# Optimization experiments

Hardware: AMD Instinct MI355X
Metric: run time of the kernel (lower is better)

Reference implementation:

```python
import jax, jax.numpy as jnp
import numpy as np

DIM = 256
HEADS = 8
WS = 7          # window size
SS = 3          # shift size
B = 16
HIMG = 56
WIMG = 56
N = WS * WS     # tokens per window = 49
HID = DIM * 4


def _rel_index(ws):
    coords = np.stack(np.meshgrid(np.arange(ws), np.arange(ws), indexing='ij')).reshape(2, -1)
    rel = (coords[:, :, None] - coords[:, None, :]).transpose(1, 2, 0)
    rel[:, :, 0] += ws - 1
    rel[:, :, 1] += ws - 1
    rel[:, :, 0] *= 2 * ws - 1
    return rel.sum(-1)  # (N, N) int

REL_IDX = jnp.asarray(_rel_index(WS))


def _make_attn_mask(H, W, ws, ss):
    img = np.zeros((H, W), dtype=np.float32)
    cnt = 0
    for hs in (slice(0, -ws), slice(-ws, -ss), slice(-ss, None)):
        for wsl in (slice(0, -ws), slice(-ws, -ss), slice(-ss, None)):
            img[hs, wsl] = cnt
            cnt += 1
    mw = img.reshape(H // ws, ws, W // ws, ws).transpose(0, 2, 1, 3).reshape(-1, ws * ws)
    diff = mw[:, None, :] - mw[:, :, None]  # (nW, N, N)
    return jnp.asarray(np.where(diff != 0, -100.0, 0.0).astype(np.float32))


def _layernorm(x, g, b):
    m = jnp.mean(x, -1, keepdims=True)
    v = jnp.mean((x - m) ** 2, -1, keepdims=True)
    return (x - m) / jnp.sqrt(v + 1e-5) * g + b


def _win_part(x, ws):
    Bb, H, W, C = x.shape
    x = x.reshape(Bb, H // ws, ws, W // ws, ws, C).transpose(0, 1, 3, 2, 4, 5)
    return x.reshape(-1, ws * ws, C)  # (B*nW, N, C)


def _win_rev(w, ws, H, W):
    C = w.shape[-1]
    Bb = w.shape[0] // ((H // ws) * (W // ws))
    x = w.reshape(Bb, H // ws, W // ws, ws, ws, C).transpose(0, 1, 3, 2, 4, 5)
    return x.reshape(Bb, H, W, C)


def setup_inputs() -> dict:
    key = jax.random.key(0)
    ks = jax.random.split(key, 20)
    n = lambda k, s, sc=0.02: jax.random.normal(k, s, dtype=jnp.float32) * sc
    inp = {
        'x1': jax.random.normal(ks[0], (B, HIMG * WIMG, DIM), dtype=jnp.float32),
        'x2': jax.random.normal(ks[1], (B, HIMG * WIMG, DIM), dtype=jnp.float32),
        'x3': jax.random.normal(ks[2], (B, HIMG * WIMG, DIM), dtype=jnp.float32),
        'attn_mask': _make_attn_mask(HIMG, WIMG, WS, SS),
        'g1': jnp.ones((DIM,), jnp.float32), 'bb1': jnp.zeros((DIM,), jnp.float32),
        'wq': n(ks[3], (DIM, DIM)), 'bq': jnp.zeros((DIM,), jnp.float32),
        'wk': n(ks[4], (DIM, DIM)), 'bk': jnp.zeros((DIM,), jnp.float32),
        'wv': n(ks[5], (DIM, DIM)), 'bv': jnp.zeros((DIM,), jnp.float32),
        'rel_table': n(ks[6], ((2 * WS - 1) ** 2, HEADS)),
        'wp': n(ks[7], (DIM, DIM)), 'bp': jnp.zeros((DIM,), jnp.float32),
        'g2': jnp.ones((DIM,), jnp.float32), 'bb2': jnp.zeros((DIM,), jnp.float32),
        'fw1': n(ks[8], (DIM, HID)), 'fb1': jnp.zeros((HID,), jnp.float32),
        'fw2': n(ks[9], (HID, DIM)), 'fb2': jnp.zeros((DIM,), jnp.float32),
        'H': HIMG, 'W': WIMG,
    }
    return inp


def reference(x1, x2, x3, attn_mask, g1, bb1, wq, bq, wk, bk, wv, bv, rel_table,
              wp, bp, g2, bb2, fw1, fb1, fw2, fb2, H, W):
    Bb, L, C = x1.shape
    hd = C // HEADS
    shortcut = x1

    def prep(x):
        x = _layernorm(x, g1, bb1).reshape(Bb, H, W, C)
        return jnp.roll(x, (-SS, -SS), axis=(1, 2))  # cyclic shift (shift_size>0)

    xw1 = _win_part(prep(x1), WS)  # (B*nW, N, C)
    xw2 = _win_part(prep(x2), WS)
    xw3 = _win_part(prep(x3), WS)

    def to_heads(x, w, b):
        y = x @ w + b
        return y.reshape(-1, N, HEADS, hd).transpose(0, 2, 1, 3)  # (B_, h, N, hd)

    q = to_heads(xw1, wq, bq) * (hd ** -0.5)
    k = to_heads(xw2, wk, bk)
    v = to_heads(xw3, wv, bv)

    attn = jnp.einsum('bhnd,bhmd->bhnm', q, k)  # (B_, h, N, N)
    bias = rel_table[REL_IDX].transpose(2, 0, 1)  # (h, N, N) gather
    attn = attn + bias[None]
    nW = attn_mask.shape[0]
    attn = attn.reshape(Bb, nW, HEADS, N, N) + attn_mask[None, :, None]
    attn = jax.nn.softmax(attn.reshape(-1, HEADS, N, N), axis=-1)

    out = jnp.einsum('bhnm,bhmd->bhnd', attn, v).transpose(0, 2, 1, 3).reshape(-1, N, C)
    out = out @ wp + bp

    x = _win_rev(out, WS, H, W)
    x = jnp.roll(x, (SS, SS), axis=(1, 2)).reshape(Bb, L, C)  # reverse shift

    x = shortcut + x
    h = jax.nn.gelu(_layernorm(x, g2, bb2) @ fw1 + fb1, approximate=False) @ fw2 + fb2
    return x + h
```

## Files before the change

### kernel.cpp

```cpp
#include <hip/hip_runtime.h>

typedef unsigned short u16;
typedef short bf16x8 __attribute__((ext_vector_type(8)));
typedef float f32x4 __attribute__((ext_vector_type(4)));

__device__ __forceinline__ u16 f2bf(float f) {
  union { float f; unsigned u; } x; x.f = f;
  unsigned r = x.u + 0x7FFFu + ((x.u >> 16) & 1u);
  return (u16)(r >> 16);
}
__device__ __forceinline__ float gelu_f(float x) {
  float t = 0.7978845608028654f * x * (1.f + 0.044715f * x * x);
  return x / (1.f + __expf(-2.f * t));
}
__device__ __forceinline__ void gll16(const void* g, void* l) {
  __builtin_amdgcn_global_load_lds(
      (const __attribute__((address_space(1))) unsigned int*)g,
      (__attribute__((address_space(3))) unsigned int*)l, 16, 0, 0);
}
__device__ __forceinline__ size_t winmap(int t) {
  int win = t / 49, i = t - win * 49;
  int b = win >> 6, wi = win & 63;
  int ih = i / 7, iw = i - ih * 7;
  int h2 = (wi >> 3) * 7 + ih + 3; if (h2 >= 56) h2 -= 56;
  int w2 = (wi & 7) * 7 + iw + 3; if (w2 >= 56) w2 -= 56;
  return ((size_t)b * 3136 + (size_t)h2 * 56 + w2) * 256;
}

__global__ __launch_bounds__(256)
void prep_all(const float* __restrict__ wq, const float* __restrict__ wk,
              const float* __restrict__ wv, const float* __restrict__ wp,
              const float* __restrict__ fw1, const float* __restrict__ fw2,
              u16* __restrict__ wqt, u16* __restrict__ wkt,
              u16* __restrict__ wvt, u16* __restrict__ wpt,
              u16* __restrict__ fw1t, u16* __restrict__ fw2t,
              const float* __restrict__ rel, const float* __restrict__ mask,
              float* __restrict__ Bp) {
  const int bx = blockIdx.x;
  const int tid = threadIdx.x;
  if (bx >= 192) {
    const int blk = bx - 192;
    const int wi = blk >> 3, h = blk & 7;
    const float* mrow = mask + (size_t)wi * 2401;
    float* ob = Bp + (size_t)blk * 4096;
#pragma unroll
    for (int e = 0; e < 16; ++e) {
      int pos = e * 256 + tid;
      int r = pos & 3, lane = (pos >> 2) & 63, mini = pos >> 8;
      int mi = mini >> 2, ni = mini & 3;
      int row = mi * 16 + (lane >> 4) * 4 + r;
      int col = ni * 16 + (lane & 15);
      float val;
      if (col >= 49) val = -1e30f;
      else if (row >= 49) val = 0.f;
      else {
        int idx = (row / 7 - col / 7 + 6) * 13 + (row % 7 - col % 7 + 6);
        val = rel[idx * 8 + h] + mrow[row * 49 + col];
      }
      ob[pos] = val;
    }
    return;
  }
  const float* in; u16* out; int K, N, t;
  if (bx < 64) {
    int j = bx >> 4; t = bx & 15; K = 256; N = 256;
    in = j == 0 ? wq : (j == 1 ? wk : (j == 2 ? wv : wp));
    out = j == 0 ? wqt : (j == 1 ? wkt : (j == 2 ? wvt : wpt));
  } else if (bx < 128) {
    t = bx - 64; in = fw1; out = fw1t; K = 256; N = 1024;
  } else {
    t = bx - 128; in = fw2; out = fw2t; K = 1024; N = 256;
  }
  const int ntn = N >> 6;
  const int tk = t / ntn, tn = t - tk * ntn;
  __shared__ u16 tile[64][72];
#pragma unroll
  for (int it = 0; it < 4; ++it) {
    int G = it * 256 + tid;
    int kk = G >> 4, gg = G & 15;
    float4 v = *(const float4*)(in + (size_t)(tk * 64 + kk) * N + tn * 64 + gg * 4);
    tile[kk][gg * 4 + 0] = f2bf(v.x);
    tile[kk][gg * 4 + 1] = f2bf(v.y);
    tile[kk][gg * 4 + 2] = f2bf(v.z);
    tile[kk][gg * 4 + 3] = f2bf(v.w);
  }
  __syncthreads();
#pragma unroll
  for (int it = 0; it < 4; ++it) {
    int G = it * 256 + tid;
    int nn = G >> 4, gk = G & 15;
    ushort4 o;
    o.x = tile[gk * 4 + 0][nn];
    o.y = tile[gk * 4 + 1][nn];
    o.z = tile[gk * 4 + 2][nn];
    o.w = tile[gk * 4 + 3][nn];
    *(ushort4*)(out + (size_t)(tn * 64 + nn) * K + tk * 64 + gk * 4) = o;
  }
}

template <int EPI, int QKV>
__global__ __launch_bounds__(256, 4)
void gemm_k256(const float* __restrict__ X0, const float* __restrict__ X1,
               const float* __restrict__ X2, const float* __restrict__ lng,
               const float* __restrict__ lnb, const u16* __restrict__ Abf,
               const u16* __restrict__ Bt, const float* __restrict__ b0,
               const float* __restrict__ b1, const float* __restrict__ b2,
               float alpha, int NC, int N, void* __restrict__ out_,
               const float* __restrict__ res) {
  __shared__ __align__(16) u16 Bl[2][32 * 256];
  const int tid = threadIdx.x, lane = tid & 63, wave = tid >> 6;
  const int q = lane >> 4, m = lane & 15;
  const int wm = wave >> 1, wn = wave & 1;
  const float* bias = b0;
  float al = alpha;
  size_t aoff = 0;
  const float* xsrc = X0;
  if constexpr (QKV) {
    const int y = blockIdx.y;
    aoff = (size_t)y * 12845056;
    Bt += (size_t)y * 65536;
    bias = (y == 0) ? b0 : (y == 1 ? b1 : b2);
    if (y) al = 1.f;
    xsrc = (y == 0) ? X0 : (y == 1 ? X1 : X2);
  }
  const long rowBase = (long)blockIdx.x * 64;

  bf16x8 af[2][8];
  if constexpr (QKV) {
    u16* Abuf = (u16*)Bl;
    const float4 gv = *(const float4*)(lng + lane * 4);
    const float4 bv = *(const float4*)(lnb + lane * 4);
#pragma unroll
    for (int pp = 0; pp < 16; ++pp) {
      int lrow = wave * 16 + pp;
      size_t src = winmap((int)(rowBase + lrow));
      float4 v = *(const float4*)(xsrc + src + lane * 4);
      float sm = v.x + v.y + v.z + v.w;
      float s2 = v.x * v.x + v.y * v.y + v.z * v.z + v.w * v.w;
#pragma unroll
      for (int d = 32; d > 0; d >>= 1) {
        sm += __shfl_xor(sm, d);
        s2 += __shfl_xor(s2, d);
      }
      float mean = sm * (1.f / 256.f);
      float rstd = rsqrtf(s2 * (1.f / 256.f) - mean * mean + 1e-5f);
      ushort4 ov;
      ov.x = f2bf((v.x - mean) * rstd * gv.x + bv.x);
      ov.y = f2bf((v.y - mean) * rstd * gv.y + bv.y);
      ov.z = f2bf((v.z - mean) * rstd * gv.z + bv.z);
      ov.w = f2bf((v.w - mean) * rstd * gv.w + bv.w);
      int g = lane >> 1;
      int gs = (g & ~7) | ((g & 7) ^ (lrow & 7));
      *(ushort4*)&Abuf[lrow * 256 + gs * 8 + (lane & 1) * 4] = ov;
    }
    __syncthreads();
#pragma unroll
    for (int mt = 0; mt < 2; ++mt) {
      int row = wm * 32 + mt * 16 + m;
#pragma unroll
      for (int ks = 0; ks < 8; ++ks) {
        int g = ks * 4 + q;
        int gs = (g & ~7) | ((g & 7) ^ (row & 7));
        af[mt][ks] = *(const bf16x8*)&Abuf[row * 256 + gs * 8];
      }
    }
    __syncthreads();
  } else {
#pragma unroll
    for (int mt = 0; mt < 2; ++mt)
#pragma unroll
      for (int ks = 0; ks < 8; ++ks)
        af[mt][ks] = *(const bf16x8*)(Abf +
                                      (size_t)(rowBase + wm * 32 + mt * 16 + m) * 256 +
                                      ks * 32 + q * 8);
  }

  size_t obase2[2][4];
  if constexpr (EPI == 2) {
#pragma unroll
    for (int mt = 0; mt < 2; ++mt)
#pragma unroll
      for (int r = 0; r < 4; ++r)
        obase2[mt][r] = winmap((int)(rowBase + wm * 32 + mt * 16 + q * 4 + r));
  }

  auto stageB = [&](u16* dst, int c) {
#pragma unroll
    for (int it = 0; it < 4; ++it) {
      int G = it * 256 + tid;
      int r = G >> 5, g = G & 31;
      int gs = (g & ~7) | ((g & 7) ^ (r & 7));
      gll16(Bt + (size_t)c * 8192 + r * 256 + gs * 8, dst + G * 8);
    }
  };

  stageB(Bl[0], 0);

  for (int c = 0; c < NC; ++c) {
    __syncthreads();
    if (c + 1 < NC) stageB(Bl[(c + 1) & 1], c + 1);
    const u16* Bc = Bl[c & 1];

    f32x4 acc[2] = {};
    const int rb = wn * 16 + m;
#pragma unroll
    for (int ks = 0; ks < 8; ++ks) {
      int g = ks * 4 + q;
      int gs = (g & ~7) | ((g & 7) ^ (rb & 7));
      bf16x8 bfv = *(const bf16x8*)&Bc[rb * 256 + gs * 8];
      acc[0] = __builtin_amdgcn_mfma_f32_16x16x32_bf16(af[0][ks], bfv, acc[0], 0, 0, 0);
      acc[1] = __builtin_amdgcn_mfma_f32_16x16x32_bf16(af[1][ks], bfv, acc[1], 0, 0, 0);
    }

    const int colb = c * 32 + wn * 16 + m;
    const float bvv = bias[colb];
    if constexpr (EPI == 2) {
      float* out = (float*)out_;
#pragma unroll
      for (int mt = 0; mt < 2; ++mt)
#pragma unroll
        for (int r = 0; r < 4; ++r)
          out[obase2[mt][r] + colb] = res[obase2[mt][r] + colb] + acc[mt][r] + bvv;
    } else {
      u16* out = (u16*)out_ + aoff;
#pragma unroll
      for (int mt = 0; mt < 2; ++mt) {
        size_t rw = (size_t)(rowBase + wm * 32 + mt * 16 + q * 4) * N;
#pragma unroll
        for (int r = 0; r < 4; ++r) {
          float vv = (acc[mt][r] + bvv) * al;
          out[rw + (size_t)r * N + colb] = f2bf(vv);
        }
      }
    }
  }
}

__global__ __launch_bounds__(256, 3)
void mlp_all(const float* __restrict__ xmid, const float* __restrict__ g2,
             const float* __restrict__ bb2, const u16* __restrict__ fw1t,
             const float* __restrict__ fb1, const u16* __restrict__ fw2t,
             const float* __restrict__ fb2, float* __restrict__ out) {
  __shared__ __align__(16) u16 bufB1[32 * 256];
  __shared__ __align__(16) u16 bufB2[256 * 32];
  __shared__ __align__(16) u16 slab[4][16 * 32];
  const int tid = threadIdx.x, lane = tid & 63, wave = tid >> 6;
  const int q = lane >> 4, m = lane & 15;
  const long rowBase = (long)blockIdx.x * 64;

  bf16x8 af[8];
  {
    const float4 gv = *(const float4*)(g2 + lane * 4);
    const float4 bv = *(const float4*)(bb2 + lane * 4);
#pragma unroll
    for (int p = 0; p < 2; ++p) {
#pragma unroll
      for (int pp = 0; pp < 8; ++pp) {
        int lrow = wave * 8 + pp;
        long grow = rowBase + p * 32 + lrow;
        float4 v = *(const float4*)(xmid + grow * 256 + lane * 4);
        float sm = v.x + v.y + v.z + v.w;
        float s2 = v.x * v.x + v.y * v.y + v.z * v.z + v.w * v.w;
#pragma unroll
        for (int d = 32; d > 0; d >>= 1) {
          sm += __shfl_xor(sm, d);
          s2 += __shfl_xor(s2, d);
        }
        float mean = sm * (1.f / 256.f);
        float rstd = rsqrtf(s2 * (1.f / 256.f) - mean * mean + 1e-5f);
        ushort4 ov;
        ov.x = f2bf((v.x - mean) * rstd * gv.x + bv.x);
        ov.y = f2bf((v.y - mean) * rstd * gv.y + bv.y);
        ov.z = f2bf((v.z - mean) * rstd * gv.z + bv.z);
        ov.w = f2bf((v.w - mean) * rstd * gv.w + bv.w);
        int g = lane >> 1;
        int gs = (g & ~7) | ((g & 7) ^ (lrow & 7));
        *(ushort4*)&bufB1[lrow * 256 + gs * 8 + (lane & 1) * 4] = ov;
      }
      __syncthreads();
      if ((wave >> 1) == p) {
        int lrow = (wave & 1) * 16 + m;
#pragma unroll
        for (int ks = 0; ks < 8; ++ks) {
          int g = ks * 4 + q;
          int gs = (g & ~7) | ((g & 7) ^ (lrow & 7));
          af[ks] = *(const bf16x8*)&bufB1[lrow * 256 + gs * 8];
        }
      }
      __syncthreads();
    }
  }

  auto stageB1 = [&](int hc) {
    const u16* src = fw1t + (size_t)hc * 8192;
#pragma unroll
    for (int it = 0; it < 4; ++it) {
      int G = it * 256 + tid;
      int r = G >> 5, g = G & 31;
      int gs = (g & ~7) | ((g & 7) ^ (r & 7));
      gll16(src + r * 256 + gs * 8, bufB1 + G * 8);
    }
  };
  auto stageB2 = [&](int hc) {
#pragma unroll
    for (int it = 0; it < 4; ++it) {
      int G = it * 256 + tid;
      int n = G >> 2, g = G & 3;
      int gs = g ^ ((n >> 1) & 3);
      gll16(fw2t + (size_t)n * 1024 + hc * 32 + gs * 8, bufB2 + G * 8);
    }
  };

  stageB1(0);

  f32x4 accO[16] = {};
  u16* sl = slab[wave];

  for (int hc = 0; hc < 32; ++hc) {
    __syncthreads();
    stageB2(hc);

    f32x4 acc1[2] = {};
#pragma unroll
    for (int ks = 0; ks < 8; ++ks) {
      int g = ks * 4 + q;
      bf16x8 bfv[2];
#pragma unroll
      for (int nt = 0; nt < 2; ++nt) {
        int r = nt * 16 + m;
        int gs = (g & ~7) | ((g & 7) ^ (r & 7));
        bfv[nt] = *(const bf16x8*)&bufB1[r * 256 + gs * 8];
      }
#pragma unroll
      for (int nt = 0; nt < 2; ++nt)
        acc1[nt] = __builtin_amdgcn_mfma_f32_16x16x32_bf16(af[ks], bfv[nt], acc1[nt], 0, 0, 0);
    }
#pragma unroll
    for (int nt = 0; nt < 2; ++nt) {
      float b1 = fb1[hc * 32 + nt * 16 + m];
      int gcol = nt * 2 + (m >> 3);
#pragma unroll
      for (int r = 0; r < 4; ++r) {
        int row = q * 4 + r;
        float h = gelu_f(acc1[nt][r] + b1);
        int gs = gcol ^ ((row >> 1) & 3);
        sl[row * 32 + gs * 8 + (m & 7)] = f2bf(h);
      }
    }
    __syncthreads();
    if (hc + 1 < 32) stageB1(hc + 1);

    {
      int gsa = q ^ ((m >> 1) & 3);
      bf16x8 pa = *(const bf16x8*)&sl[m * 32 + gsa * 8];
#pragma unroll
      for (int nt = 0; nt < 16; ++nt) {
        int n = nt * 16 + m;
        int gs2 = q ^ ((n >> 1) & 3);
        bf16x8 bv2 = *(const bf16x8*)&bufB2[n * 32 + gs2 * 8];
        accO[nt] = __builtin_amdgcn_mfma_f32_16x16x32_bf16(pa, bv2, accO[nt], 0, 0, 0);
      }
    }
  }

#pragma unroll
  for (int nt = 0; nt < 16; ++nt) {
    int col = nt * 16 + m;
    float b2 = fb2[col];
#pragma unroll
    for (int r = 0; r < 4; ++r) {
      long row = rowBase + wave * 16 + q * 4 + r;
      size_t oi = (size_t)row * 256 + col;
      out[oi] = xmid[oi] + accO[nt][r] + b2;
    }
  }
}

__global__ __launch_bounds__(64)
void attn_mfma(const u16* __restrict__ q, const u16* __restrict__ k,
               const u16* __restrict__ v, const float* __restrict__ Bp,
               u16* __restrict__ out) {
  __shared__ u16 Pl[64 * 64];
  __shared__ u16 VT[32 * 64];
  const int lane = threadIdx.x;
  const int unit = blockIdx.x;
  const int win = unit >> 3, head = unit & 7;
  const size_t base = (size_t)win * 49 * 256 + head * 32;

  {
    const int key = lane;
    const u16* vp = v + base + (size_t)key * 256;
#pragma unroll
    for (int p = 0; p < 4; ++p) {
      bf16x8 vv = {};
      if (key < 49) vv = *(const bf16x8*)(vp + p * 8);
#pragma unroll
      for (int e = 0; e < 8; ++e) {
        int dim = p * 8 + e;
        int sw = (dim ^ (dim >> 3)) & 7;
        VT[dim * 64 + ((((key >> 3) ^ sw) << 3) | (key & 7))] = (u16)vv[e];
      }
    }
  }

  const f32x4* bp = (const f32x4*)(Bp + (size_t)((win & 63) * 8 + head) * 4096);
  f32x4 acc[4][4];
#pragma unroll
  for (int mi = 0; mi < 4; ++mi)
#pragma unroll
    for (int ni = 0; ni < 4; ++ni)
      acc[mi][ni] = bp[(mi * 4 + ni) * 64 + lane];

  bf16x8 qf[4], kf[4];
#pragma unroll
  for (int mi = 0; mi < 4; ++mi)
    qf[mi] = *(const bf16x8*)(q + base + (size_t)(mi * 16 + (lane & 15)) * 256 + (lane >> 4) * 8);
#pragma unroll
  for (int ni = 0; ni < 4; ++ni)
    kf[ni] = *(const bf16x8*)(k + base + (size_t)(ni * 16 + (lane & 15)) * 256 + (lane >> 4) * 8);

#pragma unroll
  for (int mi = 0; mi < 4; ++mi)
#pragma unroll
    for (int ni = 0; ni < 4; ++ni)
      acc[mi][ni] = __builtin_amdgcn_mfma_f32_16x16x32_bf16(qf[mi], kf[ni], acc[mi][ni], 0, 0, 0);

  float rinv[4][4];
#pragma unroll
  for (int mi = 0; mi < 4; ++mi) {
#pragma unroll
    for (int r = 0; r < 4; ++r) {
      float mx = fmaxf(fmaxf(acc[mi][0][r], acc[mi][1][r]),
                       fmaxf(acc[mi][2][r], acc[mi][3][r]));
#pragma unroll
      for (int off = 1; off < 16; off <<= 1) mx = fmaxf(mx, __shfl_xor(mx, off));
      float s = 0.f;
#pragma unroll
      for (int ni = 0; ni < 4; ++ni) {
        float e = __expf(acc[mi][ni][r] - mx);
        acc[mi][ni][r] = e;
        s += e;
      }
#pragma unroll
      for (int off = 1; off < 16; off <<= 1) s += __shfl_xor(s, off);
      rinv[mi][r] = 1.f / s;
    }
  }

#pragma unroll
  for (int mi = 0; mi < 4; ++mi)
#pragma unroll
    for (int ni = 0; ni < 4; ++ni)
#pragma unroll
      for (int r = 0; r < 4; ++r) {
        int row = mi * 16 + (lane >> 4) * 4 + r;
        int col = ni * 16 + (lane & 15);
        int sw = (row ^ (row >> 3)) & 7;
        Pl[row * 64 + ((((col >> 3) ^ sw) << 3) | (col & 7))] = f2bf(acc[mi][ni][r]);
      }

  f32x4 acc2[4][2] = {};
#pragma unroll
  for (int ks = 0; ks < 2; ++ks) {
    bf16x8 pa[4], vb[2];
#pragma unroll
    for (int mi = 0; mi < 4; ++mi) {
      int row = mi * 16 + (lane & 15);
      int sw = (row ^ (row >> 3)) & 7;
      pa[mi] = *(const bf16x8*)&Pl[row * 64 + (((ks * 4 + (lane >> 4)) ^ sw) << 3)];
    }
#pragma unroll
    for (int n2 = 0; n2 < 2; ++n2) {
      int dim = n2 * 16 + (lane & 15);
      int sw = (dim ^ (dim >> 3)) & 7;
      vb[n2] = *(const bf16x8*)&VT[dim * 64 + (((ks * 4 + (lane >> 4)) ^ sw) << 3)];
    }
#pragma unroll
    for (int mi = 0; mi < 4; ++mi)
#pragma unroll
      for (int n2 = 0; n2 < 2; ++n2)
        acc2[mi][n2] = __builtin_amdgcn_mfma_f32_16x16x32_bf16(pa[mi], vb[n2], acc2[mi][n2], 0, 0, 0);
  }

#pragma unroll
  for (int mi = 0; mi < 4; ++mi)
#pragma unroll
    for (int r = 0; r < 4; ++r) {
      int row = mi * 16 + (lane >> 4) * 4 + r;
      if (row < 49) {
        float rv = rinv[mi][r];
#pragma unroll
        for (int n2 = 0; n2 < 2; ++n2) {
          int col = n2 * 16 + (lane & 15);
          out[base + (size_t)row * 256 + col] = f2bf(acc2[mi][n2][r] * rv);
        }
      }
    }
}

extern "C" void kernel_launch(void* const* d_in, const int* in_sizes, int n_in,
                              void* d_out, int out_size, void* d_ws, size_t ws_size,
                              hipStream_t stream) {
  const float* x1 = (const float*)d_in[0];
  const float* x2 = (const float*)d_in[1];
  const float* x3 = (const float*)d_in[2];
  const float* amask = (const float*)d_in[3];
  const float* g1 = (const float*)d_in[4];
  const float* bb1 = (const float*)d_in[5];
  const float* wq = (const float*)d_in[6];
  const float* bq = (const float*)d_in[7];
  const float* wk = (const float*)d_in[8];
  const float* bk = (const float*)d_in[9];
  const float* wv = (const float*)d_in[10];
  const float* bvb = (const float*)d_in[11];
  const float* rel = (const float*)d_in[12];
  const float* wp = (const float*)d_in[13];
  const float* bp = (const float*)d_in[14];
  const float* g2 = (const float*)d_in[15];
  const float* bb2 = (const float*)d_in[16];
  const float* fw1 = (const float*)d_in[17];
  const float* fb1 = (const float*)d_in[18];
  const float* fw2 = (const float*)d_in[19];
  const float* fb2 = (const float*)d_in[20];

  char* wsb = (char*)d_ws;
  const size_t S = (size_t)50176 * 256 * 2;
  u16* attn_o = (u16*)(wsb + 0 * S);
  float* x_mid = (float*)(wsb + 1 * S);
  u16* qb = (u16*)(wsb + 3 * S);
  u16* kbuf = (u16*)(wsb + 4 * S);
  u16* vbuf = (u16*)(wsb + 5 * S);
  u16* wqt = (u16*)(wsb + 6 * S);
  u16* wkt = wqt + 65536;
  u16* wvt = wkt + 65536;
  u16* wpt = wvt + 65536;
  u16* fw1t = wpt + 65536;
  u16* fw2t = fw1t + 262144;
  float* Bp = (float*)(fw2t + 262144);

  prep_all<<<dim3(704), 256, 0, stream>>>(wq, wk, wv, wp, fw1, fw2, wqt, wkt,
                                          wvt, wpt, fw1t, fw2t, rel, amask, Bp);

  gemm_k256<0, 1><<<dim3(784, 3), 256, 0, stream>>>(
      x1, x2, x3, g1, bb1, nullptr, wqt, bq, bk, bvb,
      0.17677669529663687f, 8, 256, qb, nullptr);

  attn_mfma<<<dim3(8192), 64, 0, stream>>>(qb, kbuf, vbuf, Bp, attn_o);

  gemm_k256<2, 0><<<dim3(784), 256, 0, stream>>>(
      nullptr, nullptr, nullptr, nullptr, nullptr, attn_o, wpt, bp, bp, bp,
      1.0f, 8, 256, x_mid, x1);

  mlp_all<<<dim3(784), 256, 0, stream>>>(x_mid, g2, bb2, fw1t, fb1, fw2t, fb2,
                                         (float*)d_out);
}
```

Before: 306.1 us.

## Double-buffer MLP weight tiles in LDS and cut per-chunk barriers to one

The fused MLP kernel now keeps two LDS buffers for each of the fc1 and fc2 weight chunks. It prefetches chunk hc+1 with global_load_lds while chunk hc is being computed, which leaves one barrier per iteration instead of two. The LayerNorm prologue is simplified so each wave normalises its own 16 rows into the combined buffer in a single pass. LDS use per block roughly doubles, so the launch-bounds occupancy target drops from 3 to 2 blocks per CU, trading latency hiding through occupancy for explicit overlap.

```diff
diff --git a/kernel.cpp b/kernel.cpp
--- a/kernel.cpp
+++ b/kernel.cpp
@@ -236,13 +236,13 @@
   }
 }
 
-__global__ __launch_bounds__(256, 3)
+__global__ __launch_bounds__(256, 2)
 void mlp_all(const float* __restrict__ xmid, const float* __restrict__ g2,
              const float* __restrict__ bb2, const u16* __restrict__ fw1t,
              const float* __restrict__ fb1, const u16* __restrict__ fw2t,
              const float* __restrict__ fb2, float* __restrict__ out) {
-  __shared__ __align__(16) u16 bufB1[32 * 256];
-  __shared__ __align__(16) u16 bufB2[256 * 32];
+  __shared__ __align__(16) u16 bufB1[2][32 * 256];
+  __shared__ __align__(16) u16 bufB2[2][256 * 32];
   __shared__ __align__(16) u16 slab[4][16 * 32];
   const int tid = threadIdx.x, lane = tid & 63, wave = tid >> 6;
   const int q = lane >> 4, m = lane & 15;
@@ -250,75 +250,75 @@
 
   bf16x8 af[8];
   {
+    u16* Afull = (u16*)bufB1;
     const float4 gv = *(const float4*)(g2 + lane * 4);
     const float4 bv = *(const float4*)(bb2 + lane * 4);
 #pragma unroll
-    for (int p = 0; p < 2; ++p) {
-#pragma unroll
-      for (int pp = 0; pp < 8; ++pp) {
-        int lrow = wave * 8 + pp;
-        long grow = rowBase + p * 32 + lrow;
-        float4 v = *(const float4*)(xmid + grow * 256 + lane * 4);
-        float sm = v.x + v.y + v.z + v.w;
-        float s2 = v.x * v.x + v.y * v.y + v.z * v.z + v.w * v.w;
-#pragma unroll
-        for (int d = 32; d > 0; d >>= 1) {
-          sm += __shfl_xor(sm, d);
-          s2 += __shfl_xor(s2, d);
-        }
-        float mean = sm * (1.f / 256.f);
-        float rstd = rsqrtf(s2 * (1.f / 256.f) - mean * mean + 1e-5f);
-        ushort4 ov;
-        ov.x = f2bf((v.x - mean) * rstd * gv.x + bv.x);
-        ov.y = f2bf((v.y - mean) * rstd * gv.y + bv.y);
-        ov.z = f2bf((v.z - mean) * rstd * gv.z + bv.z);
-        ov.w = f2bf((v.w - mean) * rstd * gv.w + bv.w);
-        int g = lane >> 1;
-        int gs = (g & ~7) | ((g & 7) ^ (lrow & 7));
-        *(ushort4*)&bufB1[lrow * 256 + gs * 8 + (lane & 1) * 4] = ov;
-      }
-      __syncthreads();
-      if ((wave >> 1) == p) {
-        int lrow = (wave & 1) * 16 + m;
-#pragma unroll
-        for (int ks = 0; ks < 8; ++ks) {
-          int g = ks * 4 + q;
-          int gs = (g & ~7) | ((g & 7) ^ (lrow & 7));
-          af[ks] = *(const bf16x8*)&bufB1[lrow * 256 + gs * 8];
-        }
-      }
-      __syncthreads();
-    }
-  }
-
-  auto stageB1 = [&](int hc) {
+    for (int pp = 0; pp < 16; ++pp) {
+      int lrow = wave * 16 + pp;
+      float4 v = *(const float4*)(xmid + (rowBase + lrow) * 256 + lane * 4);
+      float sm = v.x + v.y + v.z + v.w;
+      float s2 = v.x * v.x + v.y * v.y + v.z * v.z + v.w * v.w;
+#pragma unroll
+      for (int d = 32; d > 0; d >>= 1) {
+        sm += __shfl_xor(sm, d);
+        s2 += __shfl_xor(s2, d);
+      }
+      float mean = sm * (1.f / 256.f);
+      float rstd = rsqrtf(s2 * (1.f / 256.f) - mean * mean + 1e-5f);
+      ushort4 ov;
+      ov.x = f2bf((v.x - mean) * rstd * gv.x + bv.x);
+      ov.y = f2bf((v.y - mean) * rstd * gv.y + bv.y);
+      ov.z = f2bf((v.z - mean) * rstd * gv.z + bv.z);
+      ov.w = f2bf((v.w - mean) * rstd * gv.w + bv.w);
+      int g = lane >> 1;
+      int gs = (g & ~7) | ((g & 7) ^ (lrow & 7));
+      *(ushort4*)&Afull[lrow * 256 + gs * 8 + (lane & 1) * 4] = ov;
+    }
+    __syncthreads();
+    int row = wave * 16 + m;
+#pragma unroll
+    for (int ks = 0; ks < 8; ++ks) {
+      int g = ks * 4 + q;
+      int gs = (g & ~7) | ((g & 7) ^ (row & 7));
+      af[ks] = *(const bf16x8*)&Afull[row * 256 + gs * 8];
+    }
+    __syncthreads();
+  }
+
+  auto stageB1 = [&](int hc, u16* dst) {
     const u16* src = fw1t + (size_t)hc * 8192;
 #pragma unroll
     for (int it = 0; it < 4; ++it) {
       int G = it * 256 + tid;
       int r = G >> 5, g = G & 31;
       int gs = (g & ~7) | ((g & 7) ^ (r & 7));
-      gll16(src + r * 256 + gs * 8, bufB1 + G * 8);
+      gll16(src + r * 256 + gs * 8, dst + G * 8);
     }
   };
-  auto stageB2 = [&](int hc) {
+  auto stageB2 = [&](int hc, u16* dst) {
 #pragma unroll
     for (int it = 0; it < 4; ++it) {
       int G = it * 256 + tid;
       int n = G >> 2, g = G & 3;
       int gs = g ^ ((n >> 1) & 3);
-      gll16(fw2t + (size_t)n * 1024 + hc * 32 + gs * 8, bufB2 + G * 8);
+      gll16(fw2t + (size_t)n * 1024 + hc * 32 + gs * 8, dst + G * 8);
     }
   };
 
-  stageB1(0);
+  stageB1(0, bufB1[0]);
+  stageB2(0, bufB2[0]);
+  __syncthreads();
 
   f32x4 accO[16] = {};
   u16* sl = slab[wave];
 
   for (int hc = 0; hc < 32; ++hc) {
-    __syncthreads();
-    stageB2(hc);
+    const int cur = hc & 1;
+    if (hc + 1 < 32) {
+      stageB1(hc + 1, bufB1[cur ^ 1]);
+      stageB2(hc + 1, bufB2[cur ^ 1]);
+    }
 
     f32x4 acc1[2] = {};
 #pragma unroll
@@ -329,7 +329,7 @@
       for (int nt = 0; nt < 2; ++nt) {
         int r = nt * 16 + m;
         int gs = (g & ~7) | ((g & 7) ^ (r & 7));
-        bfv[nt] = *(const bf16x8*)&bufB1[r * 256 + gs * 8];
+        bfv[nt] = *(const bf16x8*)&bufB1[cur][r * 256 + gs * 8];
       }
 #pragma unroll
       for (int nt = 0; nt < 2; ++nt)
@@ -347,8 +347,6 @@
         sl[row * 32 + gs * 8 + (m & 7)] = f2bf(h);
       }
     }
-    __syncthreads();
-    if (hc + 1 < 32) stageB1(hc + 1);
 
     {
       int gsa = q ^ ((m >> 1) & 3);
@@ -357,10 +355,11 @@
       for (int nt = 0; nt < 16; ++nt) {
         int n = nt * 16 + m;
         int gs2 = q ^ ((n >> 1) & 3);
-        bf16x8 bv2 = *(const bf16x8*)&bufB2[n * 32 + gs2 * 8];
+        bf16x8 bv2 = *(const bf16x8*)&bufB2[cur][n * 32 + gs2 * 8];
         accO[nt] = __builtin_amdgcn_mfma_f32_16x16x32_bf16(pa, bv2, accO[nt], 0, 0, 0);
       }
     }
+    __syncthreads();
   }
 
 #pragma unroll
```

Result: no change. 304.1 us (-0.7%).

## Fuse output projection with residual, LayerNorm and MLP into one kernel

Applied to the files above, without the earlier changes.

Merges the projection GEMM (with window reverse, shift and residual) into the MLP kernel. The residual sum now stays in LDS as bf16 instead of going through a global fp32 x_mid buffer that was written and then read back. This removes a kernel launch and the global round trip. In exchange, LDS use per block rises, so launch bounds drop to 2 blocks, and the residual is held in bf16, which loses precision in both the LayerNorm input and the final residual add.

```diff
diff --git a/kernel.cpp b/kernel.cpp
--- a/kernel.cpp
+++ b/kernel.cpp
@@ -8,6 +8,9 @@
   union { float f; unsigned u; } x; x.f = f;
   unsigned r = x.u + 0x7FFFu + ((x.u >> 16) & 1u);
   return (u16)(r >> 16);
+}
+__device__ __forceinline__ float bf2f(u16 u) {
+  union { unsigned u; float f; } x; x.u = (unsigned)u << 16; return x.f;
 }
 __device__ __forceinline__ float gelu_f(float x) {
   float t = 0.7978845608028654f * x * (1.f + 0.044715f * x * x);
@@ -98,35 +101,27 @@
   }
 }
 
-template <int EPI, int QKV>
 __global__ __launch_bounds__(256, 4)
-void gemm_k256(const float* __restrict__ X0, const float* __restrict__ X1,
-               const float* __restrict__ X2, const float* __restrict__ lng,
-               const float* __restrict__ lnb, const u16* __restrict__ Abf,
-               const u16* __restrict__ Bt, const float* __restrict__ b0,
-               const float* __restrict__ b1, const float* __restrict__ b2,
-               float alpha, int NC, int N, void* __restrict__ out_,
-               const float* __restrict__ res) {
+void gemm_qkv(const float* __restrict__ X0, const float* __restrict__ X1,
+              const float* __restrict__ X2, const float* __restrict__ lng,
+              const float* __restrict__ lnb, const u16* __restrict__ Bt,
+              const float* __restrict__ b0, const float* __restrict__ b1,
+              const float* __restrict__ b2, float alpha,
+              u16* __restrict__ out_) {
   __shared__ __align__(16) u16 Bl[2][32 * 256];
   const int tid = threadIdx.x, lane = tid & 63, wave = tid >> 6;
   const int q = lane >> 4, m = lane & 15;
   const int wm = wave >> 1, wn = wave & 1;
-  const float* bias = b0;
-  float al = alpha;
-  size_t aoff = 0;
-  const float* xsrc = X0;
-  if constexpr (QKV) {
-    const int y = blockIdx.y;
-    aoff = (size_t)y * 12845056;
-    Bt += (size_t)y * 65536;
-    bias = (y == 0) ? b0 : (y == 1 ? b1 : b2);
-    if (y) al = 1.f;
-    xsrc = (y == 0) ? X0 : (y == 1 ? X1 : X2);
-  }
+  const int y = blockIdx.y;
+  const size_t aoff = (size_t)y * 12845056;
+  Bt += (size_t)y * 65536;
+  const float* bias = (y == 0) ? b0 : (y == 1 ? b1 : b2);
+  const float al = (y == 0) ? alpha : 1.f;
+  const float* xsrc = (y == 0) ? X0 : (y == 1 ? X1 : X2);
   const long rowBase = (long)blockIdx.x * 64;
 
   bf16x8 af[2][8];
-  if constexpr (QKV) {
+  {
     u16* Abuf = (u16*)Bl;
     const float4 gv = *(const float4*)(lng + lane * 4);
     const float4 bv = *(const float4*)(lnb + lane * 4);
@@ -165,23 +160,6 @@
       }
     }
     __syncthreads();
-  } else {
-#pragma unroll
-    for (int mt = 0; mt < 2; ++mt)
-#pragma unroll
-      for (int ks = 0; ks < 8; ++ks)
-        af[mt][ks] = *(const bf16x8*)(Abf +
-                                      (size_t)(rowBase + wm * 32 + mt * 16 + m) * 256 +
-                                      ks * 32 + q * 8);
-  }
-
-  size_t obase2[2][4];
-  if constexpr (EPI == 2) {
-#pragma unroll
-    for (int mt = 0; mt < 2; ++mt)
-#pragma unroll
-      for (int r = 0; r < 4; ++r)
-        obase2[mt][r] = winmap((int)(rowBase + wm * 32 + mt * 16 + q * 4 + r));
   }
 
   auto stageB = [&](u16* dst, int c) {
@@ -196,9 +174,9 @@
 
   stageB(Bl[0], 0);
 
-  for (int c = 0; c < NC; ++c) {
+  for (int c = 0; c < 8; ++c) {
     __syncthreads();
-    if (c + 1 < NC) stageB(Bl[(c + 1) & 1], c + 1);
+    if (c + 1 < 8) stageB(Bl[(c + 1) & 1], c + 1);
     const u16* Bc = Bl[c & 1];
 
     f32x4 acc[2] = {};
@@ -214,91 +192,64 @@
 
     const int colb = c * 32 + wn * 16 + m;
     const float bvv = bias[colb];
-    if constexpr (EPI == 2) {
-      float* out = (float*)out_;
-#pragma unroll
-      for (int mt = 0; mt < 2; ++mt)
-#pragma unroll
-        for (int r = 0; r < 4; ++r)
-          out[obase2[mt][r] + colb] = res[obase2[mt][r] + colb] + acc[mt][r] + bvv;
-    } else {
-      u16* out = (u16*)out_ + aoff;
-#pragma unroll
-      for (int mt = 0; mt < 2; ++mt) {
-        size_t rw = (size_t)(rowBase + wm * 32 + mt * 16 + q * 4) * N;
-#pragma unroll
-        for (int r = 0; r < 4; ++r) {
-          float vv = (acc[mt][r] + bvv) * al;
-          out[rw + (size_t)r * N + colb] = f2bf(vv);
-        }
-      }
-    }
-  }
-}
-
-__global__ __launch_bounds__(256, 3)
-void mlp_all(const float* __restrict__ xmid, const float* __restrict__ g2,
-             const float* __restrict__ bb2, const u16* __restrict__ fw1t,
-             const float* __restrict__ fb1, const u16* __restrict__ fw2t,
-             const float* __restrict__ fb2, float* __restrict__ out) {
-  __shared__ __align__(16) u16 bufB1[32 * 256];
-  __shared__ __align__(16) u16 bufB2[256 * 32];
+    u16* out = out_ + aoff;
+#pragma unroll
+    for (int mt = 0; mt < 2; ++mt) {
+      size_t rw = (size_t)(rowBase + wm * 32 + mt * 16 + q * 4) * 256;
+#pragma unroll
+      for (int r = 0; r < 4; ++r) {
+        float vv = (acc[mt][r] + bvv) * al;
+        out[rw + (size_t)r * 256 + colb] = f2bf(vv);
+      }
+    }
+  }
+}
+
+__global__ __launch_bounds__(256, 2)
+void proj_mlp(const u16* __restrict__ attn_o, const u16* __restrict__ wpt,
+              const float* __restrict__ bpj, const float* __restrict__ x1,
+              const float* __restrict__ g2, const float* __restrict__ bb2,
+              const u16* __restrict__ fw1t, const float* __restrict__ fb1,
+              const u16* __restrict__ fw2t, const float* __restrict__ fb2,
+              float* __restrict__ out) {
+  __shared__ __align__(16) u16 xbuf[64 * 256];
+  __shared__ __align__(16) u16 Bd0[32 * 256];
+  __shared__ __align__(16) u16 Bd1[256 * 32];
   __shared__ __align__(16) u16 slab[4][16 * 32];
   const int tid = threadIdx.x, lane = tid & 63, wave = tid >> 6;
   const int q = lane >> 4, m = lane & 15;
   const long rowBase = (long)blockIdx.x * 64;
 
-  bf16x8 af[8];
+  size_t obaseP[4];
+#pragma unroll
+  for (int r = 0; r < 4; ++r)
+    obaseP[r] = winmap((int)(rowBase + wave * 16 + q * 4 + r));
+
+  bf16x8 afP[8];
   {
-    const float4 gv = *(const float4*)(g2 + lane * 4);
-    const float4 bv = *(const float4*)(bb2 + lane * 4);
-#pragma unroll
-    for (int p = 0; p < 2; ++p) {
-#pragma unroll
-      for (int pp = 0; pp < 8; ++pp) {
-        int lrow = wave * 8 + pp;
-        long grow = rowBase + p * 32 + lrow;
-        float4 v = *(const float4*)(xmid + grow * 256 + lane * 4);
-        float sm = v.x + v.y + v.z + v.w;
-        float s2 = v.x * v.x + v.y * v.y + v.z * v.z + v.w * v.w;
-#pragma unroll
-        for (int d = 32; d > 0; d >>= 1) {
-          sm += __shfl_xor(sm, d);
-          s2 += __shfl_xor(s2, d);
-        }
-        float mean = sm * (1.f / 256.f);
-        float rstd = rsqrtf(s2 * (1.f / 256.f) - mean * mean + 1e-5f);
-        ushort4 ov;
-        ov.x = f2bf((v.x - mean) * rstd * gv.x + bv.x);
-        ov.y = f2bf((v.y - mean) * rstd * gv.y + bv.y);
-        ov.z = f2bf((v.z - mean) * rstd * gv.z + bv.z);
-        ov.w = f2bf((v.w - mean) * rstd * gv.w + bv.w);
-        int g = lane >> 1;
-        int gs = (g & ~7) | ((g & 7) ^ (lrow & 7));
-        *(ushort4*)&bufB1[lrow * 256 + gs * 8 + (lane & 1) * 4] = ov;
-      }
-      __syncthreads();
-      if ((wave >> 1) == p) {
-        int lrow = (wave & 1) * 16 + m;
-#pragma unroll
-        for (int ks = 0; ks < 8; ++ks) {
-          int g = ks * 4 + q;
-          int gs = (g & ~7) | ((g & 7) ^ (lrow & 7));
-          af[ks] = *(const bf16x8*)&bufB1[lrow * 256 + gs * 8];
-        }
-      }
-      __syncthreads();
-    }
-  }
-
-  auto stageB1 = [&](int hc) {
-    const u16* src = fw1t + (size_t)hc * 8192;
+    const u16* ap = attn_o + (size_t)(rowBase + wave * 16 + m) * 256 + q * 8;
+#pragma unroll
+    for (int ks = 0; ks < 8; ++ks) afP[ks] = *(const bf16x8*)(ap + ks * 32);
+  }
+
+  auto stageW = [&](int c, u16* dst) {
+    const u16* src = wpt + (size_t)c * 8192;
 #pragma unroll
     for (int it = 0; it < 4; ++it) {
       int G = it * 256 + tid;
       int r = G >> 5, g = G & 31;
       int gs = (g & ~7) | ((g & 7) ^ (r & 7));
-      gll16(src + r * 256 + gs * 8, bufB1 + G * 8);
+      gll16(src + r * 256 + gs * 8, dst + G * 8);
+    }
+  };
+  auto stageB1 = [&](int hc) {
+    const u16* src = fw1t + (size_t)hc * 8192;
+#pragma unroll
+    for (int it = 0; it < 4; ++it) {
+      int G = it * 256 + tid;
+      int r = G >> 5, g = G & 31;
+      int gs = (g & ~7) | ((g & 7) ^ (r & 7));
+      gll16(src + r * 256 + gs * 8, Bd0 + G * 8);
     }
   };
   auto stageB2 = [&](int hc) {
@@ -307,11 +258,88 @@
       int G = it * 256 + tid;
       int n = G >> 2, g = G & 3;
       int gs = g ^ ((n >> 1) & 3);
-      gll16(fw2t + (size_t)n * 1024 + hc * 32 + gs * 8, bufB2 + G * 8);
+      gll16(fw2t + (size_t)n * 1024 + hc * 32 + gs * 8, Bd1 + G * 8);
     }
   };
 
+  stageW(0, Bd0);
+  for (int c = 0; c < 8; ++c) {
+    __syncthreads();
+    if (c + 1 < 8) stageW(c + 1, (c & 1) ? Bd0 : Bd1);
+    const u16* Bc = (c & 1) ? Bd1 : Bd0;
+
+    f32x4 acc1[2] = {};
+#pragma unroll
+    for (int ks = 0; ks < 8; ++ks) {
+      int g = ks * 4 + q;
+      bf16x8 bfv[2];
+#pragma unroll
+      for (int nt = 0; nt < 2; ++nt) {
+        int rb = nt * 16 + m;
+        int gs = (g & ~7) | ((g & 7) ^ (rb & 7));
+        bfv[nt] = *(const bf16x8*)&Bc[rb * 256 + gs * 8];
+      }
+#pragma unroll
+      for (int nt = 0; nt < 2; ++nt)
+        acc1[nt] = __builtin_amdgcn_mfma_f32_16x16x32_bf16(afP[ks], bfv[nt], acc1[nt], 0, 0, 0);
+    }
+#pragma unroll
+    for (int nt = 0; nt < 2; ++nt) {
+      int col = c * 32 + nt * 16 + m;
+      float bvv = bpj[col];
+      int g = col >> 3;
+#pragma unroll
+      for (int r = 0; r < 4; ++r) {
+        int row = wave * 16 + q * 4 + r;
+        float v = acc1[nt][r] + bvv + x1[obaseP[r] + col];
+        int gs = (g & ~7) | ((g & 7) ^ (row & 7));
+        xbuf[row * 256 + gs * 8 + (col & 7)] = f2bf(v);
+      }
+    }
+  }
   stageB1(0);
+
+  float meanK = 0.f, rstdK = 0.f;
+#pragma unroll
+  for (int rr = 0; rr < 16; ++rr) {
+    int row = wave * 16 + rr;
+    ushort4 xv = *(const ushort4*)&xbuf[row * 256 + lane * 4];
+    float a0 = bf2f(xv.x), a1 = bf2f(xv.y), a2 = bf2f(xv.z), a3 = bf2f(xv.w);
+    float s = a0 + a1 + a2 + a3;
+    float s2 = a0 * a0 + a1 * a1 + a2 * a2 + a3 * a3;
+#pragma unroll
+    for (int d = 32; d > 0; d >>= 1) {
+      s += __shfl_xor(s, d);
+      s2 += __shfl_xor(s2, d);
+    }
+    float mean = s * (1.f / 256.f);
+    float rstd = rsqrtf(s2 * (1.f / 256.f) - mean * mean + 1e-5f);
+    if ((lane & 15) == rr) { meanK = mean; rstdK = rstd; }
+  }
+  bf16x8 af[8];
+  {
+    int row = wave * 16 + m;
+#pragma unroll
+    for (int ks = 0; ks < 8; ++ks) {
+      int g = ks * 4 + q;
+      int gs = (g & ~7) | ((g & 7) ^ (row & 7));
+      bf16x8 xv = *(const bf16x8*)&xbuf[row * 256 + gs * 8];
+      float4 ga = *(const float4*)(g2 + ks * 32 + q * 8);
+      float4 gb = *(const float4*)(g2 + ks * 32 + q * 8 + 4);
+      float4 ba = *(const float4*)(bb2 + ks * 32 + q * 8);
+      float4 bb = *(const float4*)(bb2 + ks * 32 + q * 8 + 4);
+      bf16x8 o;
+      o[0] = (short)f2bf((bf2f((u16)xv[0]) - meanK) * rstdK * ga.x + ba.x);
+      o[1] = (short)f2bf((bf2f((u16)xv[1]) - meanK) * rstdK * ga.y + ba.y);
+      o[2] = (short)f2bf((bf2f((u16)xv[2]) - meanK) * rstdK * ga.z + ba.z);
+      o[3] = (short)f2bf((bf2f((u16)xv[3]) - meanK) * rstdK * ga.w + ba.w);
+      o[4] = (short)f2bf((bf2f((u16)xv[4]) - meanK) * rstdK * gb.x + bb.x);
+      o[5] = (short)f2bf((bf2f((u16)xv[5]) - meanK) * rstdK * gb.y + bb.y);
+      o[6] = (short)f2bf((bf2f((u16)xv[6]) - meanK) * rstdK * gb.z + bb.z);
+      o[7] = (short)f2bf((bf2f((u16)xv[7]) - meanK) * rstdK * gb.w + bb.w);
+      af[ks] = o;
+    }
+  }
 
   f32x4 accO[16] = {};
   u16* sl = slab[wave];
@@ -329,7 +357,7 @@
       for (int nt = 0; nt < 2; ++nt) {
         int r = nt * 16 + m;
         int gs = (g & ~7) | ((g & 7) ^ (r & 7));
-        bfv[nt] = *(const bf16x8*)&bufB1[r * 256 + gs * 8];
+        bfv[nt] = *(const bf16x8*)&Bd0[r * 256 + gs * 8];
       }
 #pragma unroll
       for (int nt = 0; nt < 2; ++nt)
@@ -357,7 +385,7 @@
       for (int nt = 0; nt < 16; ++nt) {
         int n = nt * 16 + m;
         int gs2 = q ^ ((n >> 1) & 3);
-        bf16x8 bv2 = *(const bf16x8*)&bufB2[n * 32 + gs2 * 8];
+        bf16x8 bv2 = *(const bf16x8*)&Bd1[n * 32 + gs2 * 8];
         accO[nt] = __builtin_amdgcn_mfma_f32_16x16x32_bf16(pa, bv2, accO[nt], 0, 0, 0);
       }
     }
@@ -367,11 +395,13 @@
   for (int nt = 0; nt < 16; ++nt) {
     int col = nt * 16 + m;
     float b2 = fb2[col];
+    int g = col >> 3;
 #pragma unroll
     for (int r = 0; r < 4; ++r) {
-      long row = rowBase + wave * 16 + q * 4 + r;
-      size_t oi = (size_t)row * 256 + col;
-      out[oi] = xmid[oi] + accO[nt][r] + b2;
+      int row = wave * 16 + q * 4 + r;
+      int gs = (g & ~7) | ((g & 7) ^ (row & 7));
+      float xv = bf2f(xbuf[row * 256 + gs * 8 + (col & 7)]);
+      out[obaseP[r] + col] = xv + accO[nt][r] + b2;
     }
   }
 }
@@ -526,7 +556,6 @@
   char* wsb = (char*)d_ws;
   const size_t S = (size_t)50176 * 256 * 2;
   u16* attn_o = (u16*)(wsb + 0 * S);
-  float* x_mid = (float*)(wsb + 1 * S);
   u16* qb = (u16*)(wsb + 3 * S);
   u16* kbuf = (u16*)(wsb + 4 * S);
   u16* vbuf = (u16*)(wsb + 5 * S);
@@ -541,16 +570,12 @@
   prep_all<<<dim3(704), 256, 0, stream>>>(wq, wk, wv, wp, fw1, fw2, wqt, wkt,
                                           wvt, wpt, fw1t, fw2t, rel, amask, Bp);
 
-  gemm_k256<0, 1><<<dim3(784, 3), 256, 0, stream>>>(
-      x1, x2, x3, g1, bb1, nullptr, wqt, bq, bk, bvb,
-      0.17677669529663687f, 8, 256, qb, nullptr);
+  gemm_qkv<<<dim3(784, 3), 256, 0, stream>>>(
+      x1, x2, x3, g1, bb1, wqt, bq, bk, bvb, 0.17677669529663687f, qb);
 
   attn_mfma<<<dim3(8192), 64, 0, stream>>>(qb, kbuf, vbuf, Bp, attn_o);
 
-  gemm_k256<2, 0><<<dim3(784), 256, 0, stream>>>(
-      nullptr, nullptr, nullptr, nullptr, nullptr, attn_o, wpt, bp, bp, bp,
-      1.0f, 8, 256, x_mid, x1);
-
-  mlp_all<<<dim3(784), 256, 0, stream>>>(x_mid, g2, bb2, fw1t, fb1, fw2t, fb2,
-                                         (float*)d_out);
-}
+  proj_mlp<<<dim3(784), 256, 0, stream>>>(attn_o, wpt, bp, x1, g2, bb2,
+                                          fw1t, fb1, fw2t, fb2,
+                                          (float*)d_out);
+}
```

Result: faster. 257.9 us (median of 6 runs) (-15.7%).
